# Kernel optimization log

Hardware: AMD Instinct MI355X
Metric: run time of the kernel (lower is better)

Reference implementation:

```python
import jax, jax.numpy as jnp
import numpy as np
import math

N_HEAD = 16

def _rope(x):
    # x: [B, H, T, D], D even; interleaved-pair rotation as in the torch code
    B, H, T, D = x.shape
    theta = 10000.0 ** (-2.0 * jnp.arange(D // 2, dtype=x.dtype) / D)  # [D/2]
    pos = jnp.arange(T, dtype=x.dtype)[:, None]                        # [T,1]
    ang = pos * theta[None, :]                                          # [T, D/2]
    sin, cos = jnp.sin(ang), jnp.cos(ang)
    x1, x2 = x[..., ::2], x[..., 1::2]
    x1r = x1 * cos - x2 * sin
    x2r = x1 * sin + x2 * cos
    # re-interleave
    out = jnp.stack([x1r, x2r], axis=-1).reshape(B, H, T, D)
    return out

def setup_inputs() -> dict:
    key = jax.random.key(0)
    ks = jax.random.split(key, 3)
    B, T, C = 4, 2048, 1024
    x = jax.random.normal(ks[0], (B, T, C), dtype=jnp.float32)
    W_qkv = jax.random.normal(ks[1], (C, 3 * C), dtype=jnp.float32) * (1.0 / math.sqrt(C))
    b_qkv = jnp.zeros((3 * C,), dtype=jnp.float32)
    W_proj = jax.random.normal(ks[2], (C, C), dtype=jnp.float32) * (1.0 / math.sqrt(C))
    b_proj = jnp.zeros((C,), dtype=jnp.float32)
    return {"x": x, "W_qkv": W_qkv, "b_qkv": b_qkv, "W_proj": W_proj, "b_proj": b_proj}

def reference(x, W_qkv, b_qkv, W_proj, b_proj):
    B, T, C = x.shape
    H = N_HEAD
    D = C // H
    qkv = x @ W_qkv + b_qkv                      # [B,T,3C]
    q, k, v = jnp.split(qkv, 3, axis=-1)
    def to_heads(t):
        return t.reshape(B, T, H, D).transpose(0, 2, 1, 3)  # [B,H,T,D]
    q, k, v = to_heads(q), to_heads(k), to_heads(v)
    q = _rope(q)
    k = _rope(k)
    att = jnp.einsum('bhqd,bhkd->bhqk', q, k) * (1.0 / math.sqrt(D))
    mask = jnp.tril(jnp.ones((T, T), dtype=bool))
    att = jnp.where(mask[None, None, :, :], att, -jnp.inf)
    att = jax.nn.softmax(att, axis=-1)
    y = jnp.einsum('bhqk,bhkd->bhqd', att, v)    # [B,H,T,D]
    y = y.transpose(0, 2, 1, 3).reshape(B, T, C)
    return y @ W_proj + b_proj
```

## Files before the change

### kernel.cpp

```cpp
#include <hip/hip_runtime.h>
#include <cstddef>

#define B_DIM 4
#define T_DIM 2048
#define C_DIM 1024
#define H_DIM 16
#define D_DIM 64
#define C3_DIM 3072

typedef __attribute__((ext_vector_type(8))) __bf16 bf16x8;
typedef __attribute__((ext_vector_type(4))) __bf16 bf16x4;
typedef __attribute__((ext_vector_type(2))) __bf16 bf16x2;
typedef __attribute__((ext_vector_type(4))) float f32x4;

__global__ __launch_bounds__(256) void cvt_bf16(const float* __restrict__ in,
                                                __bf16* __restrict__ out)
{
    int i = (blockIdx.x * 256 + threadIdx.x) * 4;
    float4 v = *(const float4*)&in[i];
    bf16x4 o = { (__bf16)v.x, (__bf16)v.y, (__bf16)v.z, (__bf16)v.w };
    *(bf16x4*)&out[i] = o;
}

__global__ __launch_bounds__(256) void transpose_cvt(
    const float* __restrict__ W, __bf16* __restrict__ Wt, int K, int N)
{
    __shared__ float tile[64][65];
    const int tid = threadIdx.x;
    const int n0 = blockIdx.x * 64, k0 = blockIdx.y * 64;
    const int tx = tid & 15, ty = tid >> 4;
#pragma unroll
    for (int it = 0; it < 4; ++it) {
        int r = it * 16 + ty;
        *(float4*)&tile[r][tx * 4] =
            *(const float4*)&W[(size_t)(k0 + r) * N + n0 + tx * 4];
    }
    __syncthreads();
    int c = tid >> 2, t0 = (tid & 3) * 16;
    __align__(16) __bf16 tmp[16];
#pragma unroll
    for (int j = 0; j < 16; ++j) tmp[j] = (__bf16)tile[t0 + j][c];
    __bf16* o = Wt + (size_t)(n0 + c) * K + k0 + t0;
    *(bf16x8*)o = *(bf16x8*)&tmp[0];
    *(bf16x8*)(o + 8) = *(bf16x8*)&tmp[8];
}

template <bool OUT_BF16>
__global__ __launch_bounds__(256) void gemm_bt(
    const __bf16* __restrict__ A, const __bf16* __restrict__ Bt,
    const float* __restrict__ bias, void* __restrict__ Cout,
    int M, int N, int K)
{
    __shared__ __align__(16) __bf16 Af[8][64][8];
    __shared__ __align__(16) __bf16 Bf[8][64][8];
    const int tid = threadIdx.x;
    const int lane = tid & 63, w = tid >> 6;
    const int lm = lane & 15, lq = lane >> 4;
    const int wm = w >> 1, wn = w & 1;
    const int m0 = blockIdx.y * 128, n0 = blockIdx.x * 128;

    const __bf16* a0 = A + (size_t)(m0 + w * 32 + lm) * K + lq * 8;
    const __bf16* a1 = a0 + (size_t)16 * K;
    const __bf16* b0 = Bt + (size_t)(n0 + w * 32 + lm) * K + lq * 8;
    const __bf16* b1 = b0 + (size_t)16 * K;

    f32x4 acc[4][4];
#pragma unroll
    for (int i = 0; i < 4; ++i)
#pragma unroll
        for (int j = 0; j < 4; ++j) acc[i][j] = (f32x4){0.f, 0.f, 0.f, 0.f};

    bf16x8 ra0 = *(const bf16x8*)a0;
    bf16x8 ra1 = *(const bf16x8*)a1;
    bf16x8 rb0 = *(const bf16x8*)b0;
    bf16x8 rb1 = *(const bf16x8*)b1;

    for (int k0 = 0; k0 < K; k0 += 32) {
        __syncthreads();
        *(bf16x8*)&Af[w * 2 + 0][lane][0] = ra0;
        *(bf16x8*)&Af[w * 2 + 1][lane][0] = ra1;
        *(bf16x8*)&Bf[w * 2 + 0][lane][0] = rb0;
        *(bf16x8*)&Bf[w * 2 + 1][lane][0] = rb1;
        __syncthreads();

        int kn = (k0 + 32 < K) ? k0 + 32 : 0;
        ra0 = *(const bf16x8*)(a0 + kn);
        ra1 = *(const bf16x8*)(a1 + kn);
        rb0 = *(const bf16x8*)(b0 + kn);
        rb1 = *(const bf16x8*)(b1 + kn);

        bf16x8 av[4], bv[4];
#pragma unroll
        for (int i = 0; i < 4; ++i) {
            av[i] = *(const bf16x8*)&Af[wm * 4 + i][lane][0];
            bv[i] = *(const bf16x8*)&Bf[wn * 4 + i][lane][0];
        }
#pragma unroll
        for (int i = 0; i < 4; ++i)
#pragma unroll
            for (int j = 0; j < 4; ++j)
                acc[i][j] = __builtin_amdgcn_mfma_f32_16x16x32_bf16(
                    bv[j], av[i], acc[i][j], 0, 0, 0);
    }

#pragma unroll
    for (int i = 0; i < 4; ++i) {
        size_t row = (size_t)(m0 + wm * 64 + i * 16 + lm);
#pragma unroll
        for (int j = 0; j < 4; ++j) {
            int col = n0 + wn * 64 + j * 16 + lq * 4;
            float4 b4 = *(const float4*)&bias[col];
            float v0 = acc[i][j][0] + b4.x;
            float v1 = acc[i][j][1] + b4.y;
            float v2 = acc[i][j][2] + b4.z;
            float v3 = acc[i][j][3] + b4.w;
            if (OUT_BF16) {
                bf16x4 o = { (__bf16)v0, (__bf16)v1, (__bf16)v2, (__bf16)v3 };
                *(bf16x4*)&((__bf16*)Cout)[row * N + col] = o;
            } else {
                float4 o = make_float4(v0, v1, v2, v3);
                *(float4*)&((float*)Cout)[row * N + col] = o;
            }
        }
    }
}

__global__ __launch_bounds__(256) void ropecvt(
    __bf16* qkv, __bf16* __restrict__ Kb, __bf16* __restrict__ Vt)
{
    __shared__ __bf16 vt[64][72];
    const int tid = threadIdx.x;
    const int t0 = blockIdx.x * 64;
    const int bh = blockIdx.y;
    const int b = bh >> 4, h = bh & 15;
    __bf16* base = qkv + ((size_t)(b * T_DIM + t0)) * C3_DIM + h * D_DIM;

    {
        int rr = tid >> 3, cc = (tid & 7) * 8;
#pragma unroll
        for (int it = 0; it < 2; ++it) {
            int r = it * 32 + rr;
            *(bf16x8*)&vt[r][cc] =
                *(const bf16x8*)&base[(size_t)r * C3_DIM + 2 * C_DIM + cc];
        }
    }

    const float QSCALE = 0.125f * 1.44269504089f;

#pragma unroll
    for (int p = 0; p < 8; ++p) {
        int idx = tid + p * 256;
        int tl = idx >> 5, i = idx & 31;
        float theta = exp2f(-0.41524101186f * (float)i);
        float ang = (float)(t0 + tl) * theta;
        float s, c;
        __sincosf(ang, &s, &c);
        __bf16* qp = &base[(size_t)tl * C3_DIM + 2 * i];
        float qx = (float)qp[0], qy = (float)qp[1];
        bf16x2 qo = { (__bf16)((qx * c - qy * s) * QSCALE),
                      (__bf16)((qx * s + qy * c) * QSCALE) };
        *(bf16x2*)qp = qo;
        float kx = (float)qp[C_DIM], ky = (float)qp[C_DIM + 1];
        bf16x2 ko = { (__bf16)(kx * c - ky * s), (__bf16)(kx * s + ky * c) };
        *(bf16x2*)(Kb + ((size_t)bh * T_DIM + t0 + tl) * D_DIM + 2 * i) = ko;
    }

    __syncthreads();

    int dd = tid >> 2, tc0 = (tid & 3) * 16;
    __align__(16) __bf16 tmp[16];
#pragma unroll
    for (int j = 0; j < 16; ++j) tmp[j] = vt[tc0 + j][dd];
    __bf16* vo = Vt + ((size_t)bh * D_DIM + dd) * T_DIM + t0 + tc0;
    *(bf16x8*)vo = *(bf16x8*)&tmp[0];
    *(bf16x8*)(vo + 8) = *(bf16x8*)&tmp[8];
}

__global__ __launch_bounds__(256) void attn_mfma(
    const __bf16* __restrict__ qkvb, const __bf16* __restrict__ Kb,
    const __bf16* __restrict__ Vt, __bf16* __restrict__ yb)
{
    __shared__ __align__(16) __bf16 Kf[8][64][8];
    __shared__ __align__(16) __bf16 Vf[8][64][8];
    __shared__ __align__(16) __bf16 Pb[4][16][72];

    const int tid = threadIdx.x;
    const int bh = blockIdx.x;
    const int qt = 31 - blockIdx.y;
    const int b = bh >> 4, h = bh & 15;
    const int lane = tid & 63, w = tid >> 6;
    const int m = lane & 15, qq = lane >> 4;

    const __bf16* qrow = qkvb +
        ((size_t)(b * T_DIM + qt * 64 + w * 16 + m)) * C3_DIM + h * D_DIM + qq * 8;
    bf16x8 qreg[2];
    qreg[0] = *(const bf16x8*)qrow;
    qreg[1] = *(const bf16x8*)(qrow + 32);

    float m_i = -1e30f, l_i = 0.f;
    f32x4 acc[4];
#pragma unroll
    for (int db = 0; db < 4; ++db) acc[db] = (f32x4){0.f, 0.f, 0.f, 0.f};

    const __bf16* kg0 = Kb + (size_t)bh * T_DIM * D_DIM +
                        (size_t)(w * 16 + m) * D_DIM + qq * 8;
    const __bf16* vg0 = Vt + (size_t)bh * D_DIM * T_DIM +
                        (size_t)(w * 16 + m) * T_DIM + qq * 8;

    bf16x8 kr0 = *(const bf16x8*)(kg0);
    bf16x8 kr1 = *(const bf16x8*)(kg0 + 32);
    bf16x8 vr0 = *(const bf16x8*)(vg0);
    bf16x8 vr1 = *(const bf16x8*)(vg0 + 32);

    for (int kt = 0; kt <= qt; ++kt) {
        __syncthreads();
        *(bf16x8*)&Kf[w * 2 + 0][lane][0] = kr0;
        *(bf16x8*)&Kf[w * 2 + 1][lane][0] = kr1;
        *(bf16x8*)&Vf[w * 2 + 0][lane][0] = vr0;
        *(bf16x8*)&Vf[w * 2 + 1][lane][0] = vr1;
        __syncthreads();

        int ktn = (kt < qt) ? kt + 1 : kt;
        kr0 = *(const bf16x8*)(kg0 + (size_t)ktn * 64 * D_DIM);
        kr1 = *(const bf16x8*)(kg0 + (size_t)ktn * 64 * D_DIM + 32);
        vr0 = *(const bf16x8*)(vg0 + ktn * 64);
        vr1 = *(const bf16x8*)(vg0 + ktn * 64 + 32);

        f32x4 sv[4];
#pragma unroll
        for (int nb = 0; nb < 4; ++nb) {
            f32x4 s = (f32x4){0.f, 0.f, 0.f, 0.f};
            s = __builtin_amdgcn_mfma_f32_16x16x32_bf16(
                *(const bf16x8*)&Kf[nb * 2 + 0][lane][0], qreg[0], s, 0, 0, 0);
            s = __builtin_amdgcn_mfma_f32_16x16x32_bf16(
                *(const bf16x8*)&Kf[nb * 2 + 1][lane][0], qreg[1], s, 0, 0, 0);
            sv[nb] = s;
        }

        if (kt == qt) {
            int qlocal = w * 16 + m;
#pragma unroll
            for (int nb = 0; nb < 4; ++nb) {
                int tb = nb * 16 + qq * 4;
#pragma unroll
                for (int r = 0; r < 4; ++r)
                    if (tb + r > qlocal) sv[nb][r] = -1e30f;
            }
        }

        float mt0 = fmaxf(fmaxf(sv[0][0], sv[0][1]), fmaxf(sv[0][2], sv[0][3]));
        float mt1 = fmaxf(fmaxf(sv[1][0], sv[1][1]), fmaxf(sv[1][2], sv[1][3]));
        float mt2 = fmaxf(fmaxf(sv[2][0], sv[2][1]), fmaxf(sv[2][2], sv[2][3]));
        float mt3 = fmaxf(fmaxf(sv[3][0], sv[3][1]), fmaxf(sv[3][2], sv[3][3]));
        float mt = fmaxf(fmaxf(mt0, mt1), fmaxf(mt2, mt3));
        mt = fmaxf(mt, __shfl_xor(mt, 16));
        mt = fmaxf(mt, __shfl_xor(mt, 32));
        float mnew = fmaxf(m_i, mt);
        float alpha = exp2f(m_i - mnew);
        float ll = 0.f;
#pragma unroll
        for (int nb = 0; nb < 4; ++nb) {
            float p0 = exp2f(sv[nb][0] - mnew);
            float p1 = exp2f(sv[nb][1] - mnew);
            float p2 = exp2f(sv[nb][2] - mnew);
            float p3 = exp2f(sv[nb][3] - mnew);
            sv[nb][0] = p0; sv[nb][1] = p1; sv[nb][2] = p2; sv[nb][3] = p3;
            ll += (p0 + p1) + (p2 + p3);
        }
        ll += __shfl_xor(ll, 16);
        ll += __shfl_xor(ll, 32);
        l_i = l_i * alpha + ll;
        m_i = mnew;
#pragma unroll
        for (int db = 0; db < 4; ++db) {
            acc[db][0] *= alpha; acc[db][1] *= alpha;
            acc[db][2] *= alpha; acc[db][3] *= alpha;
        }

#pragma unroll
        for (int nb = 0; nb < 4; ++nb) {
            bf16x4 pv = { (__bf16)sv[nb][0], (__bf16)sv[nb][1],
                          (__bf16)sv[nb][2], (__bf16)sv[nb][3] };
            *(bf16x4*)&Pb[w][m][nb * 16 + qq * 4] = pv;
        }

        bf16x8 pf0 = *(const bf16x8*)&Pb[w][m][0 * 32 + qq * 8];
        bf16x8 pf1 = *(const bf16x8*)&Pb[w][m][1 * 32 + qq * 8];

#pragma unroll
        for (int db = 0; db < 4; ++db) {
            acc[db] = __builtin_amdgcn_mfma_f32_16x16x32_bf16(
                *(const bf16x8*)&Vf[db * 2 + 0][lane][0], pf0, acc[db], 0, 0, 0);
            acc[db] = __builtin_amdgcn_mfma_f32_16x16x32_bf16(
                *(const bf16x8*)&Vf[db * 2 + 1][lane][0], pf1, acc[db], 0, 0, 0);
        }
    }

    float inv = 1.0f / l_i;
    __bf16* yrow = yb + (size_t)(b * T_DIM + qt * 64 + w * 16 + m) * C_DIM +
                   h * D_DIM + qq * 4;
#pragma unroll
    for (int db = 0; db < 4; ++db) {
        bf16x4 o = { (__bf16)(acc[db][0] * inv), (__bf16)(acc[db][1] * inv),
                     (__bf16)(acc[db][2] * inv), (__bf16)(acc[db][3] * inv) };
        *(bf16x4*)(yrow + db * 16) = o;
    }
}

extern "C" void kernel_launch(void* const* d_in, const int* in_sizes, int n_in,
                              void* d_out, int out_size, void* d_ws, size_t ws_size,
                              hipStream_t stream)
{
    const float* x     = (const float*)d_in[0];
    const float* Wqkv  = (const float*)d_in[1];
    const float* bqkv  = (const float*)d_in[2];
    const float* Wproj = (const float*)d_in[3];
    const float* bproj = (const float*)d_in[4];
    float* out = (float*)d_out;

    char* ws = (char*)d_ws;
    __bf16* qkvb = (__bf16*)(ws);
    __bf16* xb   = (__bf16*)(ws + 50331648ull);
    __bf16* yb   = (__bf16*)(ws + 67108864ull);
    __bf16* Kb   = (__bf16*)(ws + 83886080ull);
    __bf16* Vt   = (__bf16*)(ws + 100663296ull);
    __bf16* Wqt  = (__bf16*)(ws + 117440512ull);
    __bf16* Wpt  = (__bf16*)(ws + 123731968ull);

    dim3 blk(256);

    cvt_bf16<<<dim3((B_DIM * T_DIM * C_DIM) / 1024), blk, 0, stream>>>(x, xb);
    transpose_cvt<<<dim3(C3_DIM / 64, C_DIM / 64), blk, 0, stream>>>(
        Wqkv, Wqt, C_DIM, C3_DIM);
    transpose_cvt<<<dim3(C_DIM / 64, C_DIM / 64), blk, 0, stream>>>(
        Wproj, Wpt, C_DIM, C_DIM);

    gemm_bt<true><<<dim3(C3_DIM / 128, (B_DIM * T_DIM) / 128), blk, 0, stream>>>(
        xb, Wqt, bqkv, qkvb, B_DIM * T_DIM, C3_DIM, C_DIM);

    ropecvt<<<dim3(T_DIM / 64, B_DIM * H_DIM), blk, 0, stream>>>(qkvb, Kb, Vt);

    attn_mfma<<<dim3(B_DIM * H_DIM, T_DIM / 64), blk, 0, stream>>>(
        qkvb, Kb, Vt, yb);

    gemm_bt<false><<<dim3(C_DIM / 128, (B_DIM * T_DIM) / 128), blk, 0, stream>>>(
        yb, Wpt, bproj, out, B_DIM * T_DIM, C_DIM, C_DIM);
}
```

Before: 342.8 us.

## Use direct global-to-LDS loads and deepen GEMM K-step to 64

The GEMM kernel now loads A and B tiles straight from global memory into LDS with global_load_lds, replacing the register-staged prefetch and the explicit LDS stores. Each iteration covers 64 elements of K instead of 32, with LDS doubled and two MFMA sub-steps per barrier pair. This removes VGPR staging and halves the number of barriers. In exchange it loses the overlap the register prefetch gave between the next tile's global loads and the current tile's MFMAs, since the loads now sit between the two barriers.

```diff
diff --git a/kernel.cpp b/kernel.cpp
--- a/kernel.cpp
+++ b/kernel.cpp
@@ -13,6 +13,9 @@
 typedef __attribute__((ext_vector_type(2))) __bf16 bf16x2;
 typedef __attribute__((ext_vector_type(4))) float f32x4;
 
+typedef const __attribute__((address_space(1))) unsigned int* gptr_t;
+typedef __attribute__((address_space(3))) unsigned int* lptr_t;
+
 __global__ __launch_bounds__(256) void cvt_bf16(const float* __restrict__ in,
                                                 __bf16* __restrict__ out)
 {
@@ -51,8 +54,8 @@
     const float* __restrict__ bias, void* __restrict__ Cout,
     int M, int N, int K)
 {
-    __shared__ __align__(16) __bf16 Af[8][64][8];
-    __shared__ __align__(16) __bf16 Bf[8][64][8];
+    __shared__ __align__(16) __bf16 Af[16][64][8];
+    __shared__ __align__(16) __bf16 Bf[16][64][8];
     const int tid = threadIdx.x;
     const int lane = tid & 63, w = tid >> 6;
     const int lm = lane & 15, lq = lane >> 4;
@@ -70,37 +73,41 @@
 #pragma unroll
         for (int j = 0; j < 4; ++j) acc[i][j] = (f32x4){0.f, 0.f, 0.f, 0.f};
 
-    bf16x8 ra0 = *(const bf16x8*)a0;
-    bf16x8 ra1 = *(const bf16x8*)a1;
-    bf16x8 rb0 = *(const bf16x8*)b0;
-    bf16x8 rb1 = *(const bf16x8*)b1;
-
-    for (int k0 = 0; k0 < K; k0 += 32) {
+    for (int k0 = 0; k0 < K; k0 += 64) {
         __syncthreads();
-        *(bf16x8*)&Af[w * 2 + 0][lane][0] = ra0;
-        *(bf16x8*)&Af[w * 2 + 1][lane][0] = ra1;
-        *(bf16x8*)&Bf[w * 2 + 0][lane][0] = rb0;
-        *(bf16x8*)&Bf[w * 2 + 1][lane][0] = rb1;
+        __builtin_amdgcn_global_load_lds((gptr_t)(const void*)(a0 + k0),
+            (lptr_t)(void*)&Af[4 * w + 0][0][0], 16, 0, 0);
+        __builtin_amdgcn_global_load_lds((gptr_t)(const void*)(a0 + k0 + 32),
+            (lptr_t)(void*)&Af[4 * w + 1][0][0], 16, 0, 0);
+        __builtin_amdgcn_global_load_lds((gptr_t)(const void*)(a1 + k0),
+            (lptr_t)(void*)&Af[4 * w + 2][0][0], 16, 0, 0);
+        __builtin_amdgcn_global_load_lds((gptr_t)(const void*)(a1 + k0 + 32),
+            (lptr_t)(void*)&Af[4 * w + 3][0][0], 16, 0, 0);
+        __builtin_amdgcn_global_load_lds((gptr_t)(const void*)(b0 + k0),
+            (lptr_t)(void*)&Bf[4 * w + 0][0][0], 16, 0, 0);
+        __builtin_amdgcn_global_load_lds((gptr_t)(const void*)(b0 + k0 + 32),
+            (lptr_t)(void*)&Bf[4 * w + 1][0][0], 16, 0, 0);
+        __builtin_amdgcn_global_load_lds((gptr_t)(const void*)(b1 + k0),
+            (lptr_t)(void*)&Bf[4 * w + 2][0][0], 16, 0, 0);
+        __builtin_amdgcn_global_load_lds((gptr_t)(const void*)(b1 + k0 + 32),
+            (lptr_t)(void*)&Bf[4 * w + 3][0][0], 16, 0, 0);
         __syncthreads();
 
-        int kn = (k0 + 32 < K) ? k0 + 32 : 0;
-        ra0 = *(const bf16x8*)(a0 + kn);
-        ra1 = *(const bf16x8*)(a1 + kn);
-        rb0 = *(const bf16x8*)(b0 + kn);
-        rb1 = *(const bf16x8*)(b1 + kn);
-
-        bf16x8 av[4], bv[4];
-#pragma unroll
-        for (int i = 0; i < 4; ++i) {
-            av[i] = *(const bf16x8*)&Af[wm * 4 + i][lane][0];
-            bv[i] = *(const bf16x8*)&Bf[wn * 4 + i][lane][0];
-        }
-#pragma unroll
-        for (int i = 0; i < 4; ++i)
-#pragma unroll
-            for (int j = 0; j < 4; ++j)
-                acc[i][j] = __builtin_amdgcn_mfma_f32_16x16x32_bf16(
-                    bv[j], av[i], acc[i][j], 0, 0, 0);
+#pragma unroll
+        for (int ks = 0; ks < 2; ++ks) {
+            bf16x8 av[4], bv[4];
+#pragma unroll
+            for (int i = 0; i < 4; ++i) {
+                av[i] = *(const bf16x8*)&Af[(wm * 4 + i) * 2 + ks][lane][0];
+                bv[i] = *(const bf16x8*)&Bf[(wn * 4 + i) * 2 + ks][lane][0];
+            }
+#pragma unroll
+            for (int i = 0; i < 4; ++i)
+#pragma unroll
+                for (int j = 0; j < 4; ++j)
+                    acc[i][j] = __builtin_amdgcn_mfma_f32_16x16x32_bf16(
+                        bv[j], av[i], acc[i][j], 0, 0, 0);
+        }
     }
 
 #pragma unroll
```

New measurement: 337.7 us. Within noise of the previous version (-1.5%).

## Fuse RoPE and V transpose into QKV GEMM epilogue, merge prep kernels

Applied to the files above, without the earlier changes.

Merges the x conversion and both weight transposes into one prep launch. Moves RoPE, Q scaling and the V transpose into the QKV GEMM epilogue, which writes head-major Q/K and transposed V directly, so the separate ropecvt pass and the full qkv intermediate round-trip go away. Both GEMMs now stage tiles with global_load_lds direct-to-LDS loads instead of the register prefetch. That drops the software overlap of the next tile's loads with compute, and the V epilogue writes scattered 8-byte stores.

```diff
diff --git a/kernel.cpp b/kernel.cpp
--- a/kernel.cpp
+++ b/kernel.cpp
@@ -13,21 +13,37 @@
 typedef __attribute__((ext_vector_type(2))) __bf16 bf16x2;
 typedef __attribute__((ext_vector_type(4))) float f32x4;
 
-__global__ __launch_bounds__(256) void cvt_bf16(const float* __restrict__ in,
-                                                __bf16* __restrict__ out)
-{
-    int i = (blockIdx.x * 256 + threadIdx.x) * 4;
-    float4 v = *(const float4*)&in[i];
-    bf16x4 o = { (__bf16)v.x, (__bf16)v.y, (__bf16)v.z, (__bf16)v.w };
-    *(bf16x4*)&out[i] = o;
-}
-
-__global__ __launch_bounds__(256) void transpose_cvt(
-    const float* __restrict__ W, __bf16* __restrict__ Wt, int K, int N)
+typedef const __attribute__((address_space(1))) unsigned int* gptr_t;
+typedef __attribute__((address_space(3))) unsigned int* lptr_t;
+
+#define QSCALE 0.180336850073f
+#define NTHETA 0.41524101186f
+
+__global__ __launch_bounds__(256) void prep(
+    const float* __restrict__ x, __bf16* __restrict__ xb,
+    const float* __restrict__ Wq, __bf16* __restrict__ Wqt,
+    const float* __restrict__ Wp, __bf16* __restrict__ Wpt)
 {
     __shared__ float tile[64][65];
-    const int tid = threadIdx.x;
-    const int n0 = blockIdx.x * 64, k0 = blockIdx.y * 64;
+    const int z = blockIdx.x, tid = threadIdx.x;
+
+    if (z < 8192) {
+        size_t i = (size_t)z * 1024 + tid * 4;
+        float4 v = *(const float4*)&x[i];
+        bf16x4 o = { (__bf16)v.x, (__bf16)v.y, (__bf16)v.z, (__bf16)v.w };
+        *(bf16x4*)&xb[i] = o;
+        return;
+    }
+
+    const float* W;
+    __bf16* Wt;
+    int N, idx;
+    if (z < 8960) { W = Wq; Wt = Wqt; N = C3_DIM; idx = z - 8192; }
+    else          { W = Wp; Wt = Wpt; N = C_DIM;  idx = z - 8960; }
+    const int K = C_DIM;
+    const int nblk = N / 64;
+    const int n0 = (idx % nblk) * 64, k0 = (idx / nblk) * 64;
+
     const int tx = tid & 15, ty = tid >> 4;
 #pragma unroll
     for (int it = 0; it < 4; ++it) {
@@ -43,6 +59,134 @@
     __bf16* o = Wt + (size_t)(n0 + c) * K + k0 + t0;
     *(bf16x8*)o = *(bf16x8*)&tmp[0];
     *(bf16x8*)(o + 8) = *(bf16x8*)&tmp[8];
+}
+
+__global__ __launch_bounds__(256) void gemm_qkv(
+    const __bf16* __restrict__ A, const __bf16* __restrict__ Bt,
+    const float* __restrict__ bias,
+    __bf16* __restrict__ Qb, __bf16* __restrict__ Kb, __bf16* __restrict__ Vt)
+{
+    __shared__ __align__(16) __bf16 Af[8][64][8];
+    __shared__ __align__(16) __bf16 Bf[8][64][8];
+    const int tid = threadIdx.x;
+    const int lane = tid & 63, w = tid >> 6;
+    const int lm = lane & 15, lq = lane >> 4;
+    const int wm = w >> 1, wn = w & 1;
+    const int m0 = blockIdx.y * 128, n0 = blockIdx.x * 128;
+    const int K = C_DIM;
+
+    const __bf16* a0 = A + (size_t)(m0 + w * 32 + lm) * K + lq * 8;
+    const __bf16* a1 = a0 + (size_t)16 * K;
+    const __bf16* b0 = Bt + (size_t)(n0 + w * 32 + lm) * K + lq * 8;
+    const __bf16* b1 = b0 + (size_t)16 * K;
+
+    f32x4 acc[4][4];
+#pragma unroll
+    for (int i = 0; i < 4; ++i)
+#pragma unroll
+        for (int j = 0; j < 4; ++j) acc[i][j] = (f32x4){0.f, 0.f, 0.f, 0.f};
+
+    const bool is_v = (n0 >= 2 * C_DIM);
+
+    if (!is_v) {
+        for (int k0 = 0; k0 < K; k0 += 32) {
+            __syncthreads();
+            __builtin_amdgcn_global_load_lds((gptr_t)(const void*)(a0 + k0),
+                (lptr_t)(void*)&Af[w * 2 + 0][0][0], 16, 0, 0);
+            __builtin_amdgcn_global_load_lds((gptr_t)(const void*)(a1 + k0),
+                (lptr_t)(void*)&Af[w * 2 + 1][0][0], 16, 0, 0);
+            __builtin_amdgcn_global_load_lds((gptr_t)(const void*)(b0 + k0),
+                (lptr_t)(void*)&Bf[w * 2 + 0][0][0], 16, 0, 0);
+            __builtin_amdgcn_global_load_lds((gptr_t)(const void*)(b1 + k0),
+                (lptr_t)(void*)&Bf[w * 2 + 1][0][0], 16, 0, 0);
+            __syncthreads();
+            bf16x8 av[4], bv[4];
+#pragma unroll
+            for (int i = 0; i < 4; ++i) {
+                av[i] = *(const bf16x8*)&Af[wm * 4 + i][lane][0];
+                bv[i] = *(const bf16x8*)&Bf[wn * 4 + i][lane][0];
+            }
+#pragma unroll
+            for (int i = 0; i < 4; ++i)
+#pragma unroll
+                for (int j = 0; j < 4; ++j)
+                    acc[i][j] = __builtin_amdgcn_mfma_f32_16x16x32_bf16(
+                        bv[j], av[i], acc[i][j], 0, 0, 0);
+        }
+
+        const bool is_q = (n0 < C_DIM);
+        const float scale = is_q ? QSCALE : 1.0f;
+        __bf16* dstbase = is_q ? Qb : Kb;
+#pragma unroll
+        for (int j = 0; j < 4; ++j) {
+            int col = n0 + wn * 64 + j * 16 + lq * 4;
+            int d0 = col & 63;
+            int h = (col & (C_DIM - 1)) >> 6;
+            float4 b4 = *(const float4*)&bias[col];
+            float th0 = exp2f(-NTHETA * (float)(d0 >> 1));
+            float th1 = exp2f(-NTHETA * (float)((d0 >> 1) + 1));
+#pragma unroll
+            for (int i = 0; i < 4; ++i) {
+                int tg = m0 + wm * 64 + i * 16 + lm;
+                int bb = tg >> 11, tl = tg & (T_DIM - 1);
+                float v0 = acc[i][j][0] + b4.x;
+                float v1 = acc[i][j][1] + b4.y;
+                float v2 = acc[i][j][2] + b4.z;
+                float v3 = acc[i][j][3] + b4.w;
+                float s0, c0, s1, c1;
+                __sincosf((float)tl * th0, &s0, &c0);
+                __sincosf((float)tl * th1, &s1, &c1);
+                bf16x4 o = { (__bf16)((v0 * c0 - v1 * s0) * scale),
+                             (__bf16)((v0 * s0 + v1 * c0) * scale),
+                             (__bf16)((v2 * c1 - v3 * s1) * scale),
+                             (__bf16)((v2 * s1 + v3 * c1) * scale) };
+                *(bf16x4*)&dstbase[((size_t)(bb * 16 + h) * T_DIM + tl) * 64 + d0] = o;
+            }
+        }
+    } else {
+        for (int k0 = 0; k0 < K; k0 += 32) {
+            __syncthreads();
+            __builtin_amdgcn_global_load_lds((gptr_t)(const void*)(a0 + k0),
+                (lptr_t)(void*)&Af[w * 2 + 0][0][0], 16, 0, 0);
+            __builtin_amdgcn_global_load_lds((gptr_t)(const void*)(a1 + k0),
+                (lptr_t)(void*)&Af[w * 2 + 1][0][0], 16, 0, 0);
+            __builtin_amdgcn_global_load_lds((gptr_t)(const void*)(b0 + k0),
+                (lptr_t)(void*)&Bf[w * 2 + 0][0][0], 16, 0, 0);
+            __builtin_amdgcn_global_load_lds((gptr_t)(const void*)(b1 + k0),
+                (lptr_t)(void*)&Bf[w * 2 + 1][0][0], 16, 0, 0);
+            __syncthreads();
+            bf16x8 av[4], bv[4];
+#pragma unroll
+            for (int i = 0; i < 4; ++i) {
+                av[i] = *(const bf16x8*)&Af[wm * 4 + i][lane][0];
+                bv[i] = *(const bf16x8*)&Bf[wn * 4 + i][lane][0];
+            }
+#pragma unroll
+            for (int i = 0; i < 4; ++i)
+#pragma unroll
+                for (int j = 0; j < 4; ++j)
+                    acc[i][j] = __builtin_amdgcn_mfma_f32_16x16x32_bf16(
+                        av[i], bv[j], acc[i][j], 0, 0, 0);
+        }
+
+#pragma unroll
+        for (int i = 0; i < 4; ++i) {
+            int t4 = m0 + wm * 64 + i * 16 + lq * 4;
+            int bb = t4 >> 11, tl = t4 & (T_DIM - 1);
+#pragma unroll
+            for (int j = 0; j < 4; ++j) {
+                int col = n0 + wn * 64 + j * 16 + lm;
+                int dfull = col - 2 * C_DIM;
+                int h = dfull >> 6, d = dfull & 63;
+                float bc = bias[col];
+                bf16x4 o = { (__bf16)(acc[i][j][0] + bc),
+                             (__bf16)(acc[i][j][1] + bc),
+                             (__bf16)(acc[i][j][2] + bc),
+                             (__bf16)(acc[i][j][3] + bc) };
+                *(bf16x4*)&Vt[((size_t)(bb * 16 + h) * 64 + d) * T_DIM + tl] = o;
+            }
+        }
+    }
 }
 
 template <bool OUT_BF16>
@@ -70,24 +214,17 @@
 #pragma unroll
         for (int j = 0; j < 4; ++j) acc[i][j] = (f32x4){0.f, 0.f, 0.f, 0.f};
 
-    bf16x8 ra0 = *(const bf16x8*)a0;
-    bf16x8 ra1 = *(const bf16x8*)a1;
-    bf16x8 rb0 = *(const bf16x8*)b0;
-    bf16x8 rb1 = *(const bf16x8*)b1;
-
     for (int k0 = 0; k0 < K; k0 += 32) {
         __syncthreads();
-        *(bf16x8*)&Af[w * 2 + 0][lane][0] = ra0;
-        *(bf16x8*)&Af[w * 2 + 1][lane][0] = ra1;
-        *(bf16x8*)&Bf[w * 2 + 0][lane][0] = rb0;
-        *(bf16x8*)&Bf[w * 2 + 1][lane][0] = rb1;
+        __builtin_amdgcn_global_load_lds((gptr_t)(const void*)(a0 + k0),
+            (lptr_t)(void*)&Af[w * 2 + 0][0][0], 16, 0, 0);
+        __builtin_amdgcn_global_load_lds((gptr_t)(const void*)(a1 + k0),
+            (lptr_t)(void*)&Af[w * 2 + 1][0][0], 16, 0, 0);
+        __builtin_amdgcn_global_load_lds((gptr_t)(const void*)(b0 + k0),
+            (lptr_t)(void*)&Bf[w * 2 + 0][0][0], 16, 0, 0);
+        __builtin_amdgcn_global_load_lds((gptr_t)(const void*)(b1 + k0),
+            (lptr_t)(void*)&Bf[w * 2 + 1][0][0], 16, 0, 0);
         __syncthreads();
-
-        int kn = (k0 + 32 < K) ? k0 + 32 : 0;
-        ra0 = *(const bf16x8*)(a0 + kn);
-        ra1 = *(const bf16x8*)(a1 + kn);
-        rb0 = *(const bf16x8*)(b0 + kn);
-        rb1 = *(const bf16x8*)(b1 + kn);
 
         bf16x8 av[4], bv[4];
 #pragma unroll
@@ -125,59 +262,8 @@
     }
 }
 
-__global__ __launch_bounds__(256) void ropecvt(
-    __bf16* qkv, __bf16* __restrict__ Kb, __bf16* __restrict__ Vt)
-{
-    __shared__ __bf16 vt[64][72];
-    const int tid = threadIdx.x;
-    const int t0 = blockIdx.x * 64;
-    const int bh = blockIdx.y;
-    const int b = bh >> 4, h = bh & 15;
-    __bf16* base = qkv + ((size_t)(b * T_DIM + t0)) * C3_DIM + h * D_DIM;
-
-    {
-        int rr = tid >> 3, cc = (tid & 7) * 8;
-#pragma unroll
-        for (int it = 0; it < 2; ++it) {
-            int r = it * 32 + rr;
-            *(bf16x8*)&vt[r][cc] =
-                *(const bf16x8*)&base[(size_t)r * C3_DIM + 2 * C_DIM + cc];
-        }
-    }
-
-    const float QSCALE = 0.125f * 1.44269504089f;
-
-#pragma unroll
-    for (int p = 0; p < 8; ++p) {
-        int idx = tid + p * 256;
-        int tl = idx >> 5, i = idx & 31;
-        float theta = exp2f(-0.41524101186f * (float)i);
-        float ang = (float)(t0 + tl) * theta;
-        float s, c;
-        __sincosf(ang, &s, &c);
-        __bf16* qp = &base[(size_t)tl * C3_DIM + 2 * i];
-        float qx = (float)qp[0], qy = (float)qp[1];
-        bf16x2 qo = { (__bf16)((qx * c - qy * s) * QSCALE),
-                      (__bf16)((qx * s + qy * c) * QSCALE) };
-        *(bf16x2*)qp = qo;
-        float kx = (float)qp[C_DIM], ky = (float)qp[C_DIM + 1];
-        bf16x2 ko = { (__bf16)(kx * c - ky * s), (__bf16)(kx * s + ky * c) };
-        *(bf16x2*)(Kb + ((size_t)bh * T_DIM + t0 + tl) * D_DIM + 2 * i) = ko;
-    }
-
-    __syncthreads();
-
-    int dd = tid >> 2, tc0 = (tid & 3) * 16;
-    __align__(16) __bf16 tmp[16];
-#pragma unroll
-    for (int j = 0; j < 16; ++j) tmp[j] = vt[tc0 + j][dd];
-    __bf16* vo = Vt + ((size_t)bh * D_DIM + dd) * T_DIM + t0 + tc0;
-    *(bf16x8*)vo = *(bf16x8*)&tmp[0];
-    *(bf16x8*)(vo + 8) = *(bf16x8*)&tmp[8];
-}
-
 __global__ __launch_bounds__(256) void attn_mfma(
-    const __bf16* __restrict__ qkvb, const __bf16* __restrict__ Kb,
+    const __bf16* __restrict__ Qb, const __bf16* __restrict__ Kb,
     const __bf16* __restrict__ Vt, __bf16* __restrict__ yb)
 {
     __shared__ __align__(16) __bf16 Kf[8][64][8];
@@ -191,8 +277,8 @@
     const int lane = tid & 63, w = tid >> 6;
     const int m = lane & 15, qq = lane >> 4;
 
-    const __bf16* qrow = qkvb +
-        ((size_t)(b * T_DIM + qt * 64 + w * 16 + m)) * C3_DIM + h * D_DIM + qq * 8;
+    const __bf16* qrow = Qb +
+        ((size_t)bh * T_DIM + qt * 64 + w * 16 + m) * D_DIM + qq * 8;
     bf16x8 qreg[2];
     qreg[0] = *(const bf16x8*)qrow;
     qreg[1] = *(const bf16x8*)(qrow + 32);
@@ -319,29 +405,23 @@
     float* out = (float*)d_out;
 
     char* ws = (char*)d_ws;
-    __bf16* qkvb = (__bf16*)(ws);
-    __bf16* xb   = (__bf16*)(ws + 50331648ull);
-    __bf16* yb   = (__bf16*)(ws + 67108864ull);
-    __bf16* Kb   = (__bf16*)(ws + 83886080ull);
-    __bf16* Vt   = (__bf16*)(ws + 100663296ull);
-    __bf16* Wqt  = (__bf16*)(ws + 117440512ull);
-    __bf16* Wpt  = (__bf16*)(ws + 123731968ull);
+    __bf16* xb  = (__bf16*)(ws);
+    __bf16* yb  = (__bf16*)(ws + 16777216ull);
+    __bf16* Qb  = (__bf16*)(ws + 33554432ull);
+    __bf16* Kb  = (__bf16*)(ws + 50331648ull);
+    __bf16* Vt  = (__bf16*)(ws + 67108864ull);
+    __bf16* Wqt = (__bf16*)(ws + 83886080ull);
+    __bf16* Wpt = (__bf16*)(ws + 90177536ull);
 
     dim3 blk(256);
 
-    cvt_bf16<<<dim3((B_DIM * T_DIM * C_DIM) / 1024), blk, 0, stream>>>(x, xb);
-    transpose_cvt<<<dim3(C3_DIM / 64, C_DIM / 64), blk, 0, stream>>>(
-        Wqkv, Wqt, C_DIM, C3_DIM);
-    transpose_cvt<<<dim3(C_DIM / 64, C_DIM / 64), blk, 0, stream>>>(
-        Wproj, Wpt, C_DIM, C_DIM);
-
-    gemm_bt<true><<<dim3(C3_DIM / 128, (B_DIM * T_DIM) / 128), blk, 0, stream>>>(
-        xb, Wqt, bqkv, qkvb, B_DIM * T_DIM, C3_DIM, C_DIM);
-
-    ropecvt<<<dim3(T_DIM / 64, B_DIM * H_DIM), blk, 0, stream>>>(qkvb, Kb, Vt);
+    prep<<<dim3(9216), blk, 0, stream>>>(x, xb, Wqkv, Wqt, Wproj, Wpt);
+
+    gemm_qkv<<<dim3(C3_DIM / 128, (B_DIM * T_DIM) / 128), blk, 0, stream>>>(
+        xb, Wqt, bqkv, Qb, Kb, Vt);
 
     attn_mfma<<<dim3(B_DIM * H_DIM, T_DIM / 64), blk, 0, stream>>>(
-        qkvb, Kb, Vt, yb);
+        Qb, Kb, Vt, yb);
 
     gemm_bt<false><<<dim3(C_DIM / 128, (B_DIM * T_DIM) / 128), blk, 0, stream>>>(
         yb, Wpt, bproj, out, B_DIM * T_DIM, C_DIM, C_DIM);
```

Result: faster. 317.0 us (-7.5%).
